# Kernel tuning notes

Measured on AMD Instinct MI355X. Metric: run time of the kernel, lower is better.

## Reference

```python
import jax, jax.numpy as jnp
import numpy as np

B, N, DIM = 2, 2048, 1024
NUM_HEADS = 16
EFF = NUM_HEADS // 2          # 8 effective heads
HD = DIM // NUM_HEADS         # 64
LAMBDA_INIT = 0.8
EPS = 1e-5


def setup_inputs() -> dict:
    key = jax.random.key(0)
    ks = jax.random.split(key, 16)
    s = 0.02
    return {
        "x":  jax.random.normal(ks[0], (B, N, DIM), dtype=jnp.float32),
        "Wq": jax.random.normal(ks[1], (DIM, DIM), dtype=jnp.float32) * s,
        "bq": jnp.zeros((DIM,), dtype=jnp.float32),
        "Wk": jax.random.normal(ks[2], (DIM, DIM), dtype=jnp.float32) * s,
        "bk": jnp.zeros((DIM,), dtype=jnp.float32),
        "Wv": jax.random.normal(ks[3], (DIM, DIM), dtype=jnp.float32) * s,
        "bv": jnp.zeros((DIM,), dtype=jnp.float32),
        "Wo": jax.random.normal(ks[4], (DIM, DIM), dtype=jnp.float32) * s,
        "bo": jnp.zeros((DIM,), dtype=jnp.float32),
        "norm_w": jnp.ones((2 * HD,), dtype=jnp.float32),
        "lq1": jax.random.normal(ks[5], (HD,), dtype=jnp.float32) * 0.1,
        "lk1": jax.random.normal(ks[6], (HD,), dtype=jnp.float32) * 0.1,
        "lq2": jax.random.normal(ks[7], (HD,), dtype=jnp.float32) * 0.1,
        "lk2": jax.random.normal(ks[8], (HD,), dtype=jnp.float32) * 0.1,
    }


def reference(x, Wq, bq, Wk, bk, Wv, bv, Wo, bo, norm_w, lq1, lk1, lq2, lk2):
    scale = HD ** -0.5
    # projections (torch Linear: y = x @ W.T + b)
    q = (x @ Wq.T + bq).reshape(B, N, NUM_HEADS, HD).transpose(0, 2, 1, 3) * scale  # [B,2E,N,hd]
    k = (x @ Wk.T + bk).reshape(B, N, NUM_HEADS, HD).transpose(0, 2, 1, 3)          # [B,2E,N,hd]
    v = (x @ Wv.T + bv).reshape(B, N, EFF, 2 * HD).transpose(0, 2, 1, 3)            # [B,E,N,2hd]

    scores = jnp.einsum('bhqd,bhkd->bhqk', q, k)              # [B,2E,N,N]
    probs = jax.nn.softmax(scores, axis=-1)
    probs = probs.reshape(B, EFF, 2, N, N)                    # pair consecutive heads

    lam = jnp.exp(jnp.sum(lq1 * lk1)) - jnp.exp(jnp.sum(lq2 * lk2)) + LAMBDA_INIT
    diff = probs[:, :, 0] - lam * probs[:, :, 1]              # [B,E,N,N]

    out = jnp.einsum('behk,bekd->behd'.replace('e','h').replace('hh','h') if False else 'bhqk,bhkd->bhqd', diff, v)  # [B,E,N,2hd]
    # headwise RMSNorm over last dim (2*hd)
    out = out * jax.lax.rsqrt(jnp.mean(out * out, axis=-1, keepdims=True) + EPS) * norm_w
    out = out * (1.0 - LAMBDA_INIT)

    out = out.transpose(0, 2, 1, 3).reshape(B, N, DIM)
    return out @ Wo.T + bo
```

## Files before the change

### kernel.cpp

```cpp
#include <hip/hip_runtime.h>
#include <hip/hip_bf16.h>

#define B_   2
#define N_   2048
#define DIM_ 1024
#define HD_  64
#define DV_  128

typedef __bf16 bf16;
typedef __bf16 bf16x8 __attribute__((ext_vector_type(8)));
typedef __bf16 bf16x4 __attribute__((ext_vector_type(4)));
typedef float  floatx4 __attribute__((ext_vector_type(4)));

#if __has_builtin(__builtin_amdgcn_exp2f)
#define EXP2(x) __builtin_amdgcn_exp2f(x)
#else
#define EXP2(x) exp2f(x)
#endif

#define QSCALE 0.1803368801111244f

__device__ __forceinline__ void async16(const void* g, void* l) {
  __builtin_amdgcn_global_load_lds(
      (__attribute__((address_space(1))) void*)g,
      (__attribute__((address_space(3))) void*)l, 16, 0, 0);
}

__global__ void convert_kernel(const float* __restrict__ x,
                               const float* __restrict__ wq,
                               const float* __restrict__ wk,
                               const float* __restrict__ wv,
                               const float* __restrict__ wo,
                               bf16* __restrict__ dst) {
  const int NX = B_ * N_ * DIM_;
  const int NW = DIM_ * DIM_;
  int i = (blockIdx.x * 256 + threadIdx.x) * 4;
  const float* src;
  int off;
  if (i < NX) { src = x; off = i; }
  else {
    int j = i - NX;
    int w = j >> 20;
    off = j & (NW - 1);
    src = (w == 0) ? wq : (w == 1) ? wk : (w == 2) ? wv : wo;
  }
  float4 v = *(const float4*)(src + off);
  bf16x4 o = { (bf16)v.x, (bf16)v.y, (bf16)v.z, (bf16)v.w };
  *(bf16x4*)(dst + i) = o;
}

__global__ void lam_kernel(const float* __restrict__ lq1, const float* __restrict__ lk1,
                           const float* __restrict__ lq2, const float* __restrict__ lk2,
                           float* __restrict__ lam_out) {
  int l = threadIdx.x;
  float a = lq1[l] * lk1[l];
  float b = lq2[l] * lk2[l];
  for (int m = 1; m < 64; m <<= 1) {
    a += __shfl_xor(a, m, 64);
    b += __shfl_xor(b, m, 64);
  }
  if (l == 0) *lam_out = __expf(a) - __expf(b) + 0.8f;
}

__global__ __launch_bounds__(256) void proj_kernel(
    const bf16* __restrict__ xb, const bf16* __restrict__ wall,
    const float* __restrict__ bq, const float* __restrict__ bk,
    const float* __restrict__ bv,
    bf16* __restrict__ qo, bf16* __restrict__ ko, bf16* __restrict__ vt) {
  __shared__ __align__(16) bf16 At[128 * 64];
  __shared__ __align__(16) bf16 Bt[128 * 64];
  const int tid = threadIdx.x, lane = tid & 63, w = tid >> 6;
  const int tm = blockIdx.x, tn = blockIdx.y, z = blockIdx.z;
  const int quad = lane >> 4, l15 = lane & 15;
  const int wm = (w >> 1) * 64, wn = (w & 1) * 64;
  const bf16* Ab = xb + (long)tm * 128 * DIM_;
  const bf16* Bb = wall + (long)z * (DIM_ * DIM_) + (long)tn * 128 * DIM_;
  floatx4 zero = {0.f, 0.f, 0.f, 0.f};
  floatx4 acc[4][4];
#pragma unroll
  for (int i = 0; i < 4; ++i)
#pragma unroll
    for (int j = 0; j < 4; ++j) acc[i][j] = zero;

  for (int kb = 0; kb < DIM_ / 64; ++kb) {
    for (int idx = tid; idx < 1024; idx += 256) {
      int row = idx >> 3, ch = idx & 7, g = ch ^ (row & 7);
      async16(Ab + row * DIM_ + kb * 64 + g * 8, (char*)At + (idx - lane) * 16);
      async16(Bb + row * DIM_ + kb * 64 + g * 8, (char*)Bt + (idx - lane) * 16);
    }
    __syncthreads();
#pragma unroll
    for (int ks = 0; ks < 2; ++ks) {
      bf16x8 af[4], bfm[4];
#pragma unroll
      for (int mt = 0; mt < 4; ++mt) {
        int r = wm + mt * 16 + l15;
        af[mt] = *(const bf16x8*)&At[r * 64 + ((ks * 4 + quad) ^ (r & 7)) * 8];
      }
#pragma unroll
      for (int nt = 0; nt < 4; ++nt) {
        int r = wn + nt * 16 + l15;
        bfm[nt] = *(const bf16x8*)&Bt[r * 64 + ((ks * 4 + quad) ^ (r & 7)) * 8];
      }
#pragma unroll
      for (int mt = 0; mt < 4; ++mt)
#pragma unroll
        for (int nt = 0; nt < 4; ++nt)
          acc[mt][nt] = __builtin_amdgcn_mfma_f32_16x16x32_bf16(
              af[mt], bfm[nt], acc[mt][nt], 0, 0, 0);
    }
    __syncthreads();
  }
#pragma unroll
  for (int mt = 0; mt < 4; ++mt)
#pragma unroll
    for (int nt = 0; nt < 4; ++nt)
#pragma unroll
      for (int r = 0; r < 4; ++r) {
        int grow = tm * 128 + wm + mt * 16 + quad * 4 + r;
        int gcol = tn * 128 + wn + nt * 16 + l15;
        float v = acc[mt][nt][r];
        if (z == 0) {
          qo[(long)grow * DIM_ + gcol] = (bf16)((v + bq[gcol]) * QSCALE);
        } else if (z == 1) {
          ko[(long)grow * DIM_ + gcol] = (bf16)(v + bk[gcol]);
        } else {
          int bb = grow >> 11, key = grow & (N_ - 1);
          int e = gcol >> 7, d = gcol & 127;
          vt[(((long)(bb * 8 + e)) * DV_ + d) * N_ + key] = (bf16)(v + bv[gcol]);
        }
      }
}

__global__ __launch_bounds__(256, 2) void attn_kernel(
    const bf16* __restrict__ qb, const bf16* __restrict__ kbuf,
    const bf16* __restrict__ vt, const float* __restrict__ lamp,
    const float* __restrict__ norm_w, bf16* __restrict__ ao) {
  __shared__ __align__(16) bf16 Kt[2 * 64 * 64];
  __shared__ __align__(16) bf16 Vt[128 * 64];
  __shared__ __align__(16) bf16 Pt[4 * 16 * 64];

  const int tid = threadIdx.x, lane = tid & 63, w = tid >> 6;
  const int qt = blockIdx.x, e = blockIdx.y, b = blockIdx.z;
  const int quad = lane >> 4, l15 = lane & 15;
  floatx4 zero = {0.f, 0.f, 0.f, 0.f};

  const int qrow = qt * 64 + w * 16 + l15;
  const bf16* qrp = qb + (long)(b * N_ + qrow) * DIM_ + e * 128;
  bf16x8 qf0[2], qf1[2];
  qf0[0] = *(const bf16x8*)(qrp + quad * 8);
  qf0[1] = *(const bf16x8*)(qrp + 32 + quad * 8);
  qf1[0] = *(const bf16x8*)(qrp + 64 + quad * 8);
  qf1[1] = *(const bf16x8*)(qrp + 96 + quad * 8);

  floatx4 acc0[8], acc1[8];
#pragma unroll
  for (int i = 0; i < 8; ++i) { acc0[i] = zero; acc1[i] = zero; }
  float lp0[4] = {0.f, 0.f, 0.f, 0.f};
  float lp1[4] = {0.f, 0.f, 0.f, 0.f};

  bf16* Ptw = Pt + w * 1024;

  for (int kt = 0; kt < N_ / 64; ++kt) {
#pragma unroll
    for (int t = 0; t < 4; ++t) {
      int idx = tid + t * 256;
      int khl = idx >> 9, row = (idx >> 3) & 63, ch = idx & 7, g = ch ^ (row & 7);
      async16(kbuf + ((long)(b * N_ + kt * 64 + row)) * DIM_ + (e * 2 + khl) * 64 + g * 8,
              (char*)Kt + (idx - lane) * 16);
    }
#pragma unroll
    for (int t = 0; t < 4; ++t) {
      int idx = tid + t * 256;
      int row = idx >> 3, ch = idx & 7, g = ch ^ (row & 7);
      async16(vt + ((long)((b * 8 + e) * DV_ + row)) * N_ + kt * 64 + g * 8,
              (char*)Vt + (idx - lane) * 16);
    }
    __syncthreads();

#pragma unroll
    for (int hl = 0; hl < 2; ++hl) {
      const bf16* Kh = Kt + hl * 4096;
      floatx4* acc = hl ? acc1 : acc0;
      float* lp = hl ? lp1 : lp0;

      floatx4 s[4];
#pragma unroll
      for (int nt = 0; nt < 4; ++nt) s[nt] = zero;
#pragma unroll
      for (int ks = 0; ks < 2; ++ks) {
        bf16x8 qf = hl ? qf1[ks] : qf0[ks];
#pragma unroll
        for (int nt = 0; nt < 4; ++nt) {
          int br = nt * 16 + l15;
          bf16x8 bfm = *(const bf16x8*)&Kh[br * 64 + ((ks * 4 + quad) ^ (br & 7)) * 8];
          s[nt] = __builtin_amdgcn_mfma_f32_16x16x32_bf16(qf, bfm, s[nt], 0, 0, 0);
        }
      }

#pragma unroll
      for (int r = 0; r < 4; ++r) {
        float p0 = EXP2(s[0][r]);
        float p1 = EXP2(s[1][r]);
        float p2 = EXP2(s[2][r]);
        float p3 = EXP2(s[3][r]);
        lp[r] += (p0 + p1) + (p2 + p3);
        int row = quad * 4 + r;
        int k0 = l15;
        Ptw[row * 64 + ((k0 >> 3) ^ (row & 7)) * 8 + (k0 & 7)] = (bf16)p0;
        int k1 = 16 + l15;
        Ptw[row * 64 + ((k1 >> 3) ^ (row & 7)) * 8 + (k1 & 7)] = (bf16)p1;
        int k2 = 32 + l15;
        Ptw[row * 64 + ((k2 >> 3) ^ (row & 7)) * 8 + (k2 & 7)] = (bf16)p2;
        int k3 = 48 + l15;
        Ptw[row * 64 + ((k3 >> 3) ^ (row & 7)) * 8 + (k3 & 7)] = (bf16)p3;
      }

#pragma unroll
      for (int ks = 0; ks < 2; ++ks) {
        bf16x8 af = *(const bf16x8*)&Ptw[l15 * 64 + ((ks * 4 + quad) ^ (l15 & 7)) * 8];
#pragma unroll
        for (int dt = 0; dt < 8; ++dt) {
          int br = dt * 16 + l15;
          bf16x8 bfm = *(const bf16x8*)&Vt[br * 64 + ((ks * 4 + quad) ^ (br & 7)) * 8];
          acc[dt] = __builtin_amdgcn_mfma_f32_16x16x32_bf16(af, bfm, acc[dt], 0, 0, 0);
        }
      }
    }
    __syncthreads();
  }

  float inv0[4], inv1[4];
#pragma unroll
  for (int r = 0; r < 4; ++r) {
    float a = lp0[r], c = lp1[r];
#pragma unroll
    for (int msk = 1; msk < 16; msk <<= 1) {
      a += __shfl_xor(a, msk, 16);
      c += __shfl_xor(c, msk, 16);
    }
    inv0[r] = 1.0f / a;
    inv1[r] = 1.0f / c;
  }

  float lam = *lamp;
  float ss[4] = {0.f, 0.f, 0.f, 0.f};
#pragma unroll
  for (int dt = 0; dt < 8; ++dt)
#pragma unroll
    for (int r = 0; r < 4; ++r) {
      float v = acc0[dt][r] * inv0[r] - lam * (acc1[dt][r] * inv1[r]);
      acc0[dt][r] = v;
      ss[r] += v * v;
    }
  float rms[4];
#pragma unroll
  for (int r = 0; r < 4; ++r) {
    float t = ss[r];
#pragma unroll
    for (int msk = 1; msk < 16; msk <<= 1) t += __shfl_xor(t, msk, 16);
    rms[r] = rsqrtf(t * (1.0f / 128.0f) + 1e-5f);
  }
#pragma unroll
  for (int dt = 0; dt < 8; ++dt) {
    float nwv = norm_w[dt * 16 + l15] * 0.2f;
#pragma unroll
    for (int r = 0; r < 4; ++r) {
      int n = qt * 64 + w * 16 + quad * 4 + r;
      ao[((long)(b * N_ + n)) * DIM_ + e * DV_ + dt * 16 + l15] =
          (bf16)(acc0[dt][r] * rms[r] * nwv);
    }
  }
}

__global__ __launch_bounds__(256) void out_gemm(
    const bf16* __restrict__ ab, const bf16* __restrict__ wo,
    const float* __restrict__ bo, float* __restrict__ out) {
  __shared__ __align__(16) bf16 At[128 * 64];
  __shared__ __align__(16) bf16 Bt[128 * 64];
  const int tid = threadIdx.x, lane = tid & 63, w = tid >> 6;
  const int tm = blockIdx.x, tn = blockIdx.y;
  const int quad = lane >> 4, l15 = lane & 15;
  const int wm = (w >> 1) * 64, wn = (w & 1) * 64;
  const bf16* Ab = ab + (long)tm * 128 * DIM_;
  const bf16* Bb = wo + (long)tn * 128 * DIM_;
  floatx4 zero = {0.f, 0.f, 0.f, 0.f};
  floatx4 acc[4][4];
#pragma unroll
  for (int i = 0; i < 4; ++i)
#pragma unroll
    for (int j = 0; j < 4; ++j) acc[i][j] = zero;

  for (int kb = 0; kb < DIM_ / 64; ++kb) {
    for (int idx = tid; idx < 1024; idx += 256) {
      int row = idx >> 3, ch = idx & 7, g = ch ^ (row & 7);
      async16(Ab + row * DIM_ + kb * 64 + g * 8, (char*)At + (idx - lane) * 16);
      async16(Bb + row * DIM_ + kb * 64 + g * 8, (char*)Bt + (idx - lane) * 16);
    }
    __syncthreads();
#pragma unroll
    for (int ks = 0; ks < 2; ++ks) {
      bf16x8 af[4], bfm[4];
#pragma unroll
      for (int mt = 0; mt < 4; ++mt) {
        int r = wm + mt * 16 + l15;
        af[mt] = *(const bf16x8*)&At[r * 64 + ((ks * 4 + quad) ^ (r & 7)) * 8];
      }
#pragma unroll
      for (int nt = 0; nt < 4; ++nt) {
        int r = wn + nt * 16 + l15;
        bfm[nt] = *(const bf16x8*)&Bt[r * 64 + ((ks * 4 + quad) ^ (r & 7)) * 8];
      }
#pragma unroll
      for (int mt = 0; mt < 4; ++mt)
#pragma unroll
        for (int nt = 0; nt < 4; ++nt)
          acc[mt][nt] = __builtin_amdgcn_mfma_f32_16x16x32_bf16(
              af[mt], bfm[nt], acc[mt][nt], 0, 0, 0);
    }
    __syncthreads();
  }
#pragma unroll
  for (int mt = 0; mt < 4; ++mt)
#pragma unroll
    for (int nt = 0; nt < 4; ++nt)
#pragma unroll
      for (int r = 0; r < 4; ++r) {
        int grow = tm * 128 + wm + mt * 16 + quad * 4 + r;
        int gcol = tn * 128 + wn + nt * 16 + l15;
        out[(long)grow * DIM_ + gcol] = acc[mt][nt][r] + bo[gcol];
      }
}

extern "C" void kernel_launch(void* const* d_in, const int* in_sizes, int n_in,
                              void* d_out, int out_size, void* d_ws, size_t ws_size,
                              hipStream_t stream) {
  const float* x    = (const float*)d_in[0];
  const float* Wq   = (const float*)d_in[1];
  const float* bq   = (const float*)d_in[2];
  const float* Wk   = (const float*)d_in[3];
  const float* bk   = (const float*)d_in[4];
  const float* Wv   = (const float*)d_in[5];
  const float* bv   = (const float*)d_in[6];
  const float* Wo   = (const float*)d_in[7];
  const float* bo   = (const float*)d_in[8];
  const float* nw   = (const float*)d_in[9];
  const float* lq1  = (const float*)d_in[10];
  const float* lk1  = (const float*)d_in[11];
  const float* lq2  = (const float*)d_in[12];
  const float* lk2  = (const float*)d_in[13];

  char* ws = (char*)d_ws;
  float* lam = (float*)ws;
  bf16* xb   = (bf16*)(ws + 256);
  bf16* wqb  = xb + 4194304;
  bf16* qb   = wqb + 4 * 1048576;
  bf16* kbuf = qb + 4194304;
  bf16* vtb  = kbuf + 4194304;
  bf16* ab   = vtb + 4194304;

  convert_kernel<<<8192, 256, 0, stream>>>(x, Wq, Wk, Wv, Wo, xb);
  lam_kernel<<<1, 64, 0, stream>>>(lq1, lk1, lq2, lk2, lam);
  proj_kernel<<<dim3(32, 8, 3), 256, 0, stream>>>(xb, wqb, bq, bk, bv, qb, kbuf, vtb);
  attn_kernel<<<dim3(32, 8, 2), 256, 0, stream>>>(qb, kbuf, vtb, lam, nw, ab);
  out_gemm<<<dim3(32, 8), 256, 0, stream>>>(ab, wqb + 3 * 1048576, bo, (float*)d_out);
}
```

Measured before the change: 244.7 us.

## Double-buffer K/V tiles in attention and interleave both paired heads

Gives the K and V LDS tiles two buffers each. The next key tile's async global-to-LDS loads are issued right after the barrier, so they overlap with compute on the current tile, and one barrier per iteration is dropped. The two heads of each differential pair are now processed together in one loop body, so each V fragment read from LDS feeds two MFMAs and more independent MFMA chains are available. The cost is a larger LDS footprint (about 80KB per block, near the limit for two blocks per CU) and more live registers, which could hurt occupancy or cause spills.

```diff
diff --git a/kernel.cpp b/kernel.cpp
--- a/kernel.cpp
+++ b/kernel.cpp
@@ -136,9 +136,9 @@
     const bf16* __restrict__ qb, const bf16* __restrict__ kbuf,
     const bf16* __restrict__ vt, const float* __restrict__ lamp,
     const float* __restrict__ norm_w, bf16* __restrict__ ao) {
-  __shared__ __align__(16) bf16 Kt[2 * 64 * 64];
-  __shared__ __align__(16) bf16 Vt[128 * 64];
-  __shared__ __align__(16) bf16 Pt[4 * 16 * 64];
+  __shared__ __align__(16) bf16 Kt[2][2 * 64 * 64];
+  __shared__ __align__(16) bf16 Vt[2][128 * 64];
+  __shared__ __align__(16) bf16 Pt[4][2][16 * 64];
 
   const int tid = threadIdx.x, lane = tid & 63, w = tid >> 6;
   const int qt = blockIdx.x, e = blockIdx.y, b = blockIdx.z;
@@ -153,81 +153,92 @@
   qf1[0] = *(const bf16x8*)(qrp + 64 + quad * 8);
   qf1[1] = *(const bf16x8*)(qrp + 96 + quad * 8);
 
+  const bf16* kbase = kbuf + (long)b * N_ * DIM_ + e * 128;
+  const bf16* vbase = vt + (long)(b * 8 + e) * DV_ * N_;
+
   floatx4 acc0[8], acc1[8];
 #pragma unroll
   for (int i = 0; i < 8; ++i) { acc0[i] = zero; acc1[i] = zero; }
   float lp0[4] = {0.f, 0.f, 0.f, 0.f};
   float lp1[4] = {0.f, 0.f, 0.f, 0.f};
 
-  bf16* Ptw = Pt + w * 1024;
+  bf16* Pt0 = Pt[w][0];
+  bf16* Pt1 = Pt[w][1];
+
+#define STAGE(ktv, bufv)                                                            \
+  {                                                                                 \
+    int kt_ = (ktv), buf_ = (bufv);                                                 \
+    _Pragma("unroll") for (int t = 0; t < 4; ++t) {                                 \
+      int idx = tid + t * 256;                                                      \
+      int khl = idx >> 9, row = (idx >> 3) & 63, ch = idx & 7, g = ch ^ (row & 7);  \
+      async16(kbase + ((long)(kt_ * 64 + row)) * DIM_ + khl * 64 + g * 8,           \
+              (char*)Kt[buf_] + (idx - lane) * 16);                                 \
+    }                                                                               \
+    _Pragma("unroll") for (int t = 0; t < 4; ++t) {                                 \
+      int idx = tid + t * 256;                                                      \
+      int row = idx >> 3, ch = idx & 7, g = ch ^ (row & 7);                         \
+      async16(vbase + (long)row * N_ + kt_ * 64 + g * 8,                            \
+              (char*)Vt[buf_] + (idx - lane) * 16);                                 \
+    }                                                                               \
+  }
+
+  STAGE(0, 0);
 
   for (int kt = 0; kt < N_ / 64; ++kt) {
-#pragma unroll
-    for (int t = 0; t < 4; ++t) {
-      int idx = tid + t * 256;
-      int khl = idx >> 9, row = (idx >> 3) & 63, ch = idx & 7, g = ch ^ (row & 7);
-      async16(kbuf + ((long)(b * N_ + kt * 64 + row)) * DIM_ + (e * 2 + khl) * 64 + g * 8,
-              (char*)Kt + (idx - lane) * 16);
-    }
-#pragma unroll
-    for (int t = 0; t < 4; ++t) {
-      int idx = tid + t * 256;
-      int row = idx >> 3, ch = idx & 7, g = ch ^ (row & 7);
-      async16(vt + ((long)((b * 8 + e) * DV_ + row)) * N_ + kt * 64 + g * 8,
-              (char*)Vt + (idx - lane) * 16);
-    }
-    __syncthreads();
-
-#pragma unroll
-    for (int hl = 0; hl < 2; ++hl) {
-      const bf16* Kh = Kt + hl * 4096;
-      floatx4* acc = hl ? acc1 : acc0;
-      float* lp = hl ? lp1 : lp0;
-
-      floatx4 s[4];
-#pragma unroll
-      for (int nt = 0; nt < 4; ++nt) s[nt] = zero;
-#pragma unroll
-      for (int ks = 0; ks < 2; ++ks) {
-        bf16x8 qf = hl ? qf1[ks] : qf0[ks];
-#pragma unroll
-        for (int nt = 0; nt < 4; ++nt) {
-          int br = nt * 16 + l15;
-          bf16x8 bfm = *(const bf16x8*)&Kh[br * 64 + ((ks * 4 + quad) ^ (br & 7)) * 8];
-          s[nt] = __builtin_amdgcn_mfma_f32_16x16x32_bf16(qf, bfm, s[nt], 0, 0, 0);
-        }
-      }
-
-#pragma unroll
-      for (int r = 0; r < 4; ++r) {
-        float p0 = EXP2(s[0][r]);
-        float p1 = EXP2(s[1][r]);
-        float p2 = EXP2(s[2][r]);
-        float p3 = EXP2(s[3][r]);
-        lp[r] += (p0 + p1) + (p2 + p3);
-        int row = quad * 4 + r;
-        int k0 = l15;
-        Ptw[row * 64 + ((k0 >> 3) ^ (row & 7)) * 8 + (k0 & 7)] = (bf16)p0;
-        int k1 = 16 + l15;
-        Ptw[row * 64 + ((k1 >> 3) ^ (row & 7)) * 8 + (k1 & 7)] = (bf16)p1;
-        int k2 = 32 + l15;
-        Ptw[row * 64 + ((k2 >> 3) ^ (row & 7)) * 8 + (k2 & 7)] = (bf16)p2;
-        int k3 = 48 + l15;
-        Ptw[row * 64 + ((k3 >> 3) ^ (row & 7)) * 8 + (k3 & 7)] = (bf16)p3;
-      }
-
-#pragma unroll
-      for (int ks = 0; ks < 2; ++ks) {
-        bf16x8 af = *(const bf16x8*)&Ptw[l15 * 64 + ((ks * 4 + quad) ^ (l15 & 7)) * 8];
-#pragma unroll
-        for (int dt = 0; dt < 8; ++dt) {
-          int br = dt * 16 + l15;
-          bf16x8 bfm = *(const bf16x8*)&Vt[br * 64 + ((ks * 4 + quad) ^ (br & 7)) * 8];
-          acc[dt] = __builtin_amdgcn_mfma_f32_16x16x32_bf16(af, bfm, acc[dt], 0, 0, 0);
-        }
-      }
-    }
-    __syncthreads();
+    const int buf = kt & 1;
+    __syncthreads();
+    if (kt + 1 < N_ / 64) STAGE(kt + 1, buf ^ 1);
+
+    const bf16* Kh0 = Kt[buf];
+    const bf16* Kh1 = Kt[buf] + 4096;
+    const bf16* Vb = Vt[buf];
+
+    floatx4 s0[4], s1[4];
+#pragma unroll
+    for (int nt = 0; nt < 4; ++nt) { s0[nt] = zero; s1[nt] = zero; }
+#pragma unroll
+    for (int ks = 0; ks < 2; ++ks) {
+#pragma unroll
+      for (int nt = 0; nt < 4; ++nt) {
+        int br = nt * 16 + l15;
+        int so = ((ks * 4 + quad) ^ (br & 7)) * 8;
+        bf16x8 b0 = *(const bf16x8*)&Kh0[br * 64 + so];
+        bf16x8 b1 = *(const bf16x8*)&Kh1[br * 64 + so];
+        s0[nt] = __builtin_amdgcn_mfma_f32_16x16x32_bf16(qf0[ks], b0, s0[nt], 0, 0, 0);
+        s1[nt] = __builtin_amdgcn_mfma_f32_16x16x32_bf16(qf1[ks], b1, s1[nt], 0, 0, 0);
+      }
+    }
+
+#pragma unroll
+    for (int r = 0; r < 4; ++r) {
+      int row = quad * 4 + r;
+      int a0 = row * 64 + ((l15 >> 3) ^ (row & 7)) * 8 + (l15 & 7);
+      int a1 = row * 64 + (((16 + l15) >> 3) ^ (row & 7)) * 8 + (l15 & 7);
+      int a2 = row * 64 + (((32 + l15) >> 3) ^ (row & 7)) * 8 + (l15 & 7);
+      int a3 = row * 64 + (((48 + l15) >> 3) ^ (row & 7)) * 8 + (l15 & 7);
+      float p0 = EXP2(s0[0][r]), p1 = EXP2(s0[1][r]);
+      float p2 = EXP2(s0[2][r]), p3 = EXP2(s0[3][r]);
+      lp0[r] += (p0 + p1) + (p2 + p3);
+      Pt0[a0] = (bf16)p0; Pt0[a1] = (bf16)p1; Pt0[a2] = (bf16)p2; Pt0[a3] = (bf16)p3;
+      float u0 = EXP2(s1[0][r]), u1 = EXP2(s1[1][r]);
+      float u2 = EXP2(s1[2][r]), u3 = EXP2(s1[3][r]);
+      lp1[r] += (u0 + u1) + (u2 + u3);
+      Pt1[a0] = (bf16)u0; Pt1[a1] = (bf16)u1; Pt1[a2] = (bf16)u2; Pt1[a3] = (bf16)u3;
+    }
+
+#pragma unroll
+    for (int ks = 0; ks < 2; ++ks) {
+      int ao_ = l15 * 64 + ((ks * 4 + quad) ^ (l15 & 7)) * 8;
+      bf16x8 af0 = *(const bf16x8*)&Pt0[ao_];
+      bf16x8 af1 = *(const bf16x8*)&Pt1[ao_];
+#pragma unroll
+      for (int dt = 0; dt < 8; ++dt) {
+        int br = dt * 16 + l15;
+        bf16x8 bfm = *(const bf16x8*)&Vb[br * 64 + ((ks * 4 + quad) ^ (br & 7)) * 8];
+        acc0[dt] = __builtin_amdgcn_mfma_f32_16x16x32_bf16(af0, bfm, acc0[dt], 0, 0, 0);
+        acc1[dt] = __builtin_amdgcn_mfma_f32_16x16x32_bf16(af1, bfm, acc1[dt], 0, 0, 0);
+      }
+    }
   }
 
   float inv0[4], inv1[4];
```

After: 239.8 us. -2.0%, faster.
